# Kernel tuning notes

Hardware: AMD Instinct MI355X
Metric: run time of the kernel (lower is better)

The kernel has to match this reference:

```python
import jax, jax.numpy as jnp
import numpy as np

N_QUBITS = 8
DEPTH = 2
DIM = 2 ** N_QUBITS

# Hadamard gate (symmetric)
_H = (1.0 / np.sqrt(2.0)) * jnp.array([[1.0, 1.0], [1.0, -1.0]], dtype=jnp.complex64)
# sign table for <Z_i>: bit of wire i is bit (n-1-i) of the basis index (wire 0 = MSB)
_bits = (np.arange(DIM)[:, None] >> np.arange(N_QUBITS - 1, -1, -1)[None, :]) & 1
_SIGNS = jnp.asarray(1.0 - 2.0 * _bits, dtype=jnp.float32)  # [DIM, n_qubits]


def _quantum(ang):
    """Vectorized statevector simulation of the circuit:
    RX(ang_i) on each wire, then DEPTH x (CNOT ladder + H on last wire);
    returns <Z_i> for each wire. ang: [R, N_QUBITS] float32 -> [R, N_QUBITS]."""
    R = ang.shape[0]
    half = ang * 0.5
    a0 = jnp.cos(half).astype(jnp.complex64)
    a1 = (jnp.sin(half) * (-1j)).astype(jnp.complex64)  # RX|0> = cos|0> - i sin|1>
    single = jnp.stack([a0, a1], axis=-1)  # [R, n, 2]
    # product state via kron over qubits (wire 0 is the most significant factor)
    state = single[:, 0]  # [R, 2]
    for q in range(1, N_QUBITS):
        state = (state[:, :, None] * single[:, q][:, None, :]).reshape(R, -1)
    for _ in range(DEPTH):
        # CNOT ladder on adjacent wires (i -> i+1)
        for i in range(N_QUBITS - 1):
            s = state.reshape(R, 2 ** i, 2, 2, -1)  # [R, pre, ctrl, tgt, post]
            s = jnp.concatenate([s[:, :, :1], s[:, :, 1:, ::-1]], axis=2)
            state = s.reshape(R, -1)
        # Hadamard on the last wire
        s = state.reshape(R, -1, 2)
        state = (s @ _H).reshape(R, -1)
    probs = state.real ** 2 + state.imag ** 2  # [R, DIM]
    return probs @ _SIGNS  # [R, n_qubits]


def setup_inputs() -> dict:
    key = jax.random.key(0)
    k_x, k_w1, k_w2 = jax.random.split(key, 3)
    B, S, E, F = 8, 4096, 1024, N_QUBITS
    x = jax.random.normal(k_x, (B, S, E), dtype=jnp.float32)
    w1 = jax.random.normal(k_w1, (F, E), dtype=jnp.float32) * 0.02
    b1 = jnp.zeros((F,), dtype=jnp.float32)
    w2 = jax.random.normal(k_w2, (E, F), dtype=jnp.float32) * 0.02
    b2 = jnp.zeros((E,), dtype=jnp.float32)
    return {"x": x, "w1": w1, "b1": b1, "w2": w2, "b2": b2}


def reference(x, w1, b1, w2, b2):
    B, S, E = x.shape
    h = jnp.einsum('bse,fe->bsf', x, w1) + b1  # linear1 -> [B, S, ffn_dim]
    q = _quantum(h.reshape(-1, N_QUBITS)).reshape(B, S, N_QUBITS)
    # dropout is identity in eval mode
    return jnp.einsum('bsf,ef->bse', q, w2) + b2  # linear2 -> [B, S, E]
```

## Files before the change

kernel.cpp:

```cpp
#include <hip/hip_runtime.h>


constexpr int THREADS        = 256;
constexpr int ROWS_PER_ITER  = 8;
constexpr int ITERS          = 4;
constexpr int ROWS_PER_BLOCK = ROWS_PER_ITER * ITERS;
constexpr int E              = 1024;
constexpr int R_TOTAL        = 8 * 4096;

__global__ __launch_bounds__(THREADS)
void ffq_kernel(const float* __restrict__ x,
                const float* __restrict__ w1,
                const float* __restrict__ b1,
                const float* __restrict__ w2,
                const float* __restrict__ b2,
                float* __restrict__ out)
{
    __shared__ __align__(16) float part[2][ROWS_PER_ITER][4][8];
    __shared__ __align__(16) float qsh[2][ROWS_PER_ITER][8];
    __shared__ float b1s[8];

    const int t    = threadIdx.x;
    const int lane = t & 63;
    const int wid  = t >> 6;
    const int c0   = t * 4;

    if (t < 8) b1s[t] = b1[t];

    float4 w1r[8];
#pragma unroll
    for (int f = 0; f < 8; ++f)
        w1r[f] = *(const float4*)(w1 + f * E + c0);

    float w2a[4][8];
#pragma unroll
    for (int j = 0; j < 4; ++j) {
        const float4 lo = *(const float4*)(w2 + (size_t)(c0 + j) * 8);
        const float4 hi = *(const float4*)(w2 + (size_t)(c0 + j) * 8 + 4);
        w2a[j][0] = lo.x; w2a[j][1] = lo.y; w2a[j][2] = lo.z; w2a[j][3] = lo.w;
        w2a[j][4] = hi.x; w2a[j][5] = hi.y; w2a[j][6] = hi.z; w2a[j][7] = hi.w;
    }
    const float4 b2v = *(const float4*)(b2 + c0);

    const int row0 = blockIdx.x * ROWS_PER_BLOCK;

    float4 xv[ROWS_PER_ITER];
#pragma unroll
    for (int s = 0; s < ROWS_PER_ITER; ++s)
        xv[s] = *(const float4*)(x + (size_t)(row0 + s) * E + c0);

    for (int it = 0; it < ITERS; ++it) {
        const int p        = it & 1;
        const int rbase    = row0 + it * ROWS_PER_ITER;
        const bool hasNext = (it + 1 < ITERS);

#pragma unroll
        for (int s = 0; s < ROWS_PER_ITER; ++s) {
            const float4 xc = xv[s];
            if (hasNext)
                xv[s] = *(const float4*)(x + (size_t)(rbase + ROWS_PER_ITER + s) * E + c0);

            float h[8];
#pragma unroll
            for (int f = 0; f < 8; ++f)
                h[f] = xc.x * w1r[f].x + xc.y * w1r[f].y
                     + xc.z * w1r[f].z + xc.w * w1r[f].w;

            {   const bool hb = lane & 1;
                float s0 = hb ? h[0] : h[4];
                float s1 = hb ? h[1] : h[5];
                float s2 = hb ? h[2] : h[6];
                float s3 = hb ? h[3] : h[7];
                s0 = __shfl_xor(s0, 1); s1 = __shfl_xor(s1, 1);
                s2 = __shfl_xor(s2, 1); s3 = __shfl_xor(s3, 1);
                h[0] = (hb ? h[4] : h[0]) + s0;
                h[1] = (hb ? h[5] : h[1]) + s1;
                h[2] = (hb ? h[6] : h[2]) + s2;
                h[3] = (hb ? h[7] : h[3]) + s3;
            }
            {   const bool hb = lane & 2;
                float s0 = hb ? h[0] : h[2];
                float s1 = hb ? h[1] : h[3];
                s0 = __shfl_xor(s0, 2); s1 = __shfl_xor(s1, 2);
                h[0] = (hb ? h[2] : h[0]) + s0;
                h[1] = (hb ? h[3] : h[1]) + s1;
            }
            float v;
            {   const bool hb = lane & 4;
                float s0 = hb ? h[0] : h[1];
                s0 = __shfl_xor(s0, 4);
                v = (hb ? h[1] : h[0]) + s0;
            }
            v += __shfl_xor(v, 8);
            v += __shfl_xor(v, 16);
            v += __shfl_xor(v, 32);

            if (lane < 8) {
                const int f = ((lane & 1) << 2) | (lane & 2) | ((lane >> 2) & 1);
                part[p][s][wid][f] = v;
            }
        }
        __syncthreads();

        if (t < ROWS_PER_ITER) {
            float hq[8];
#pragma unroll
            for (int f = 0; f < 8; ++f)
                hq[f] = part[p][t][0][f] + part[p][t][1][f]
                      + part[p][t][2][f] + part[p][t][3][f] + b1s[f];
            float c[8];
#pragma unroll
            for (int f = 0; f < 8; ++f) c[f] = __cosf(hq[f]);
            const float e1 = c[0],      o1 = c[1];
            const float e2 = e1 * c[2], o2 = o1 * c[3];
            const float e3 = e2 * c[4], o3 = o2 * c[5];
            const float e4 = e3 * c[6];
            float* qp = qsh[p][t];
            qp[0] = e1; qp[1] = o1; qp[2] = e2; qp[3] = o2;
            qp[4] = e3; qp[5] = o3; qp[6] = e4; qp[7] = e4 * o3 * c[7];
        }
        __syncthreads();

#pragma unroll
        for (int s = 0; s < ROWS_PER_ITER; ++s) {
            const float4 qlo = *(const float4*)(&qsh[p][s][0]);
            const float4 qhi = *(const float4*)(&qsh[p][s][4]);
            const float qv[8] = {qlo.x, qlo.y, qlo.z, qlo.w,
                                 qhi.x, qhi.y, qhi.z, qhi.w};
            float4 o = b2v;
#pragma unroll
            for (int f = 0; f < 8; ++f) {
                o.x += qv[f] * w2a[0][f];
                o.y += qv[f] * w2a[1][f];
                o.z += qv[f] * w2a[2][f];
                o.w += qv[f] * w2a[3][f];
            }
            *(float4*)(out + (size_t)(rbase + s) * E + c0) = o;
        }
    }
}

extern "C" void kernel_launch(void* const* d_in, const int* in_sizes, int n_in,
                              void* d_out, int out_size, void* d_ws, size_t ws_size,
                              hipStream_t stream)
{
    const float* x  = (const float*)d_in[0];
    const float* w1 = (const float*)d_in[1];
    const float* b1 = (const float*)d_in[2];
    const float* w2 = (const float*)d_in[3];
    const float* b2 = (const float*)d_in[4];
    float* out = (float*)d_out;

    dim3 grid(R_TOTAL / ROWS_PER_BLOCK);
    ffq_kernel<<<grid, THREADS, 0, stream>>>(x, w1, b1, w2, b2, out);
}
```

Measured before the change: 249.5 us.

## Split fused kernel into read-reduce-cosine kernel and output-projection kernel

The single fused kernel is split in two. The first kernel streams x, computes the 8 projections and the cosine products, and writes the small q tensor to workspace. The second kernel reads q and writes the full output. The goal is to separate the read-bound phase from the write-bound phase so neither waits on the other's barriers. The cosine products are now computed in parallel across lanes with shuffle prefix products, where before a handful of threads did them. The cost is a second launch and a small round trip through global memory for q.

```diff
diff --git a/kernel.cpp b/kernel.cpp
--- a/kernel.cpp
+++ b/kernel.cpp
@@ -1,36 +1,107 @@
 #include <hip/hip_runtime.h>
 
 
-constexpr int THREADS        = 256;
-constexpr int ROWS_PER_ITER  = 8;
-constexpr int ITERS          = 4;
-constexpr int ROWS_PER_BLOCK = ROWS_PER_ITER * ITERS;
-constexpr int E              = 1024;
-constexpr int R_TOTAL        = 8 * 4096;
+constexpr int E       = 1024;
+constexpr int R_TOTAL = 8 * 4096;
+constexpr int ROWS_A  = 32;
+constexpr int ROWS_B  = 16;
 
-__global__ __launch_bounds__(THREADS)
-void ffq_kernel(const float* __restrict__ x,
-                const float* __restrict__ w1,
-                const float* __restrict__ b1,
-                const float* __restrict__ w2,
-                const float* __restrict__ b2,
-                float* __restrict__ out)
+__global__ __launch_bounds__(256)
+void ffq_qkernel(const float* __restrict__ x,
+                 const float* __restrict__ w1,
+                 const float* __restrict__ b1,
+                 float* __restrict__ q)
 {
-    __shared__ __align__(16) float part[2][ROWS_PER_ITER][4][8];
-    __shared__ __align__(16) float qsh[2][ROWS_PER_ITER][8];
-    __shared__ float b1s[8];
+    __shared__ float part[ROWS_A][33];
 
     const int t    = threadIdx.x;
     const int lane = t & 63;
     const int wid  = t >> 6;
     const int c0   = t * 4;
 
-    if (t < 8) b1s[t] = b1[t];
-
     float4 w1r[8];
 #pragma unroll
     for (int f = 0; f < 8; ++f)
         w1r[f] = *(const float4*)(w1 + f * E + c0);
+
+    const int row0 = blockIdx.x * ROWS_A;
+
+    float4 xv = *(const float4*)(x + (size_t)row0 * E + c0);
+    for (int s = 0; s < ROWS_A; ++s) {
+        const float4 xc = xv;
+        if (s + 1 < ROWS_A)
+            xv = *(const float4*)(x + (size_t)(row0 + s + 1) * E + c0);
+
+        float h[8];
+#pragma unroll
+        for (int f = 0; f < 8; ++f)
+            h[f] = xc.x * w1r[f].x + xc.y * w1r[f].y
+                 + xc.z * w1r[f].z + xc.w * w1r[f].w;
+
+        {   const bool hb = lane & 1;
+            float s0 = hb ? h[0] : h[4];
+            float s1 = hb ? h[1] : h[5];
+            float s2 = hb ? h[2] : h[6];
+            float s3 = hb ? h[3] : h[7];
+            s0 = __shfl_xor(s0, 1); s1 = __shfl_xor(s1, 1);
+            s2 = __shfl_xor(s2, 1); s3 = __shfl_xor(s3, 1);
+            h[0] = (hb ? h[4] : h[0]) + s0;
+            h[1] = (hb ? h[5] : h[1]) + s1;
+            h[2] = (hb ? h[6] : h[2]) + s2;
+            h[3] = (hb ? h[7] : h[3]) + s3;
+        }
+        {   const bool hb = lane & 2;
+            float s0 = hb ? h[0] : h[2];
+            float s1 = hb ? h[1] : h[3];
+            s0 = __shfl_xor(s0, 2); s1 = __shfl_xor(s1, 2);
+            h[0] = (hb ? h[2] : h[0]) + s0;
+            h[1] = (hb ? h[3] : h[1]) + s1;
+        }
+        float v;
+        {   const bool hb = lane & 4;
+            float s0 = hb ? h[0] : h[1];
+            s0 = __shfl_xor(s0, 4);
+            v = (hb ? h[1] : h[0]) + s0;
+        }
+        v += __shfl_xor(v, 8);
+        v += __shfl_xor(v, 16);
+        v += __shfl_xor(v, 32);
+
+        if (lane < 8) {
+            const int f = ((lane & 1) << 2) | (lane & 2) | ((lane >> 2) & 1);
+            part[s][f * 4 + wid] = v;
+        }
+    }
+    __syncthreads();
+
+    {
+        const int s = wid * 8 + (lane >> 3);
+        const int f = lane & 7;
+        const float hq = part[s][f * 4 + 0] + part[s][f * 4 + 1]
+                       + part[s][f * 4 + 2] + part[s][f * 4 + 3] + b1[f];
+        float p = __cosf(hq);
+        float u = __shfl_up(p, 2, 8); if (f >= 2) p *= u;
+        u = __shfl_up(p, 4, 8);       if (f >= 4) p *= u;
+        const float p6 = __shfl(p, 6, 8);
+        if (f == 7) p *= p6;
+        q[(size_t)(row0 + s) * 8 + f] = p;
+    }
+}
+
+__global__ __launch_bounds__(256)
+void ffq_okernel(const float* __restrict__ q,
+                 const float* __restrict__ w2,
+                 const float* __restrict__ b2,
+                 float* __restrict__ out)
+{
+    __shared__ __align__(16) float4 qsh[ROWS_B * 2];
+
+    const int t  = threadIdx.x;
+    const int c0 = t * 4;
+    const int row0 = blockIdx.x * ROWS_B;
+
+    if (t < ROWS_B * 2)
+        qsh[t] = ((const float4*)(q + (size_t)row0 * 8))[t];
 
     float w2a[4][8];
 #pragma unroll
@@ -42,101 +113,23 @@
     }
     const float4 b2v = *(const float4*)(b2 + c0);
 
-    const int row0 = blockIdx.x * ROWS_PER_BLOCK;
+    __syncthreads();
 
-    float4 xv[ROWS_PER_ITER];
+#pragma unroll 4
+    for (int s = 0; s < ROWS_B; ++s) {
+        const float4 qlo = qsh[2 * s];
+        const float4 qhi = qsh[2 * s + 1];
+        const float qv[8] = {qlo.x, qlo.y, qlo.z, qlo.w,
+                             qhi.x, qhi.y, qhi.z, qhi.w};
+        float4 o = b2v;
 #pragma unroll
-    for (int s = 0; s < ROWS_PER_ITER; ++s)
-        xv[s] = *(const float4*)(x + (size_t)(row0 + s) * E + c0);
-
-    for (int it = 0; it < ITERS; ++it) {
-        const int p        = it & 1;
-        const int rbase    = row0 + it * ROWS_PER_ITER;
-        const bool hasNext = (it + 1 < ITERS);
-
-#pragma unroll
-        for (int s = 0; s < ROWS_PER_ITER; ++s) {
-            const float4 xc = xv[s];
-            if (hasNext)
-                xv[s] = *(const float4*)(x + (size_t)(rbase + ROWS_PER_ITER + s) * E + c0);
-
-            float h[8];
-#pragma unroll
-            for (int f = 0; f < 8; ++f)
-                h[f] = xc.x * w1r[f].x + xc.y * w1r[f].y
-                     + xc.z * w1r[f].z + xc.w * w1r[f].w;
-
-            {   const bool hb = lane & 1;
-                float s0 = hb ? h[0] : h[4];
-                float s1 = hb ? h[1] : h[5];
-                float s2 = hb ? h[2] : h[6];
-                float s3 = hb ? h[3] : h[7];
-                s0 = __shfl_xor(s0, 1); s1 = __shfl_xor(s1, 1);
-                s2 = __shfl_xor(s2, 1); s3 = __shfl_xor(s3, 1);
-                h[0] = (hb ? h[4] : h[0]) + s0;
-                h[1] = (hb ? h[5] : h[1]) + s1;
-                h[2] = (hb ? h[6] : h[2]) + s2;
-                h[3] = (hb ? h[7] : h[3]) + s3;
-            }
-            {   const bool hb = lane & 2;
-                float s0 = hb ? h[0] : h[2];
-                float s1 = hb ? h[1] : h[3];
-                s0 = __shfl_xor(s0, 2); s1 = __shfl_xor(s1, 2);
-                h[0] = (hb ? h[2] : h[0]) + s0;
-                h[1] = (hb ? h[3] : h[1]) + s1;
-            }
-            float v;
-            {   const bool hb = lane & 4;
-                float s0 = hb ? h[0] : h[1];
-                s0 = __shfl_xor(s0, 4);
-                v = (hb ? h[1] : h[0]) + s0;
-            }
-            v += __shfl_xor(v, 8);
-            v += __shfl_xor(v, 16);
-            v += __shfl_xor(v, 32);
-
-            if (lane < 8) {
-                const int f = ((lane & 1) << 2) | (lane & 2) | ((lane >> 2) & 1);
-                part[p][s][wid][f] = v;
-            }
+        for (int f = 0; f < 8; ++f) {
+            o.x += qv[f] * w2a[0][f];
+            o.y += qv[f] * w2a[1][f];
+            o.z += qv[f] * w2a[2][f];
+            o.w += qv[f] * w2a[3][f];
         }
-        __syncthreads();
-
-        if (t < ROWS_PER_ITER) {
-            float hq[8];
-#pragma unroll
-            for (int f = 0; f < 8; ++f)
-                hq[f] = part[p][t][0][f] + part[p][t][1][f]
-                      + part[p][t][2][f] + part[p][t][3][f] + b1s[f];
-            float c[8];
-#pragma unroll
-            for (int f = 0; f < 8; ++f) c[f] = __cosf(hq[f]);
-            const float e1 = c[0],      o1 = c[1];
-            const float e2 = e1 * c[2], o2 = o1 * c[3];
-            const float e3 = e2 * c[4], o3 = o2 * c[5];
-            const float e4 = e3 * c[6];
-            float* qp = qsh[p][t];
-            qp[0] = e1; qp[1] = o1; qp[2] = e2; qp[3] = o2;
-            qp[4] = e3; qp[5] = o3; qp[6] = e4; qp[7] = e4 * o3 * c[7];
-        }
-        __syncthreads();
-
-#pragma unroll
-        for (int s = 0; s < ROWS_PER_ITER; ++s) {
-            const float4 qlo = *(const float4*)(&qsh[p][s][0]);
-            const float4 qhi = *(const float4*)(&qsh[p][s][4]);
-            const float qv[8] = {qlo.x, qlo.y, qlo.z, qlo.w,
-                                 qhi.x, qhi.y, qhi.z, qhi.w};
-            float4 o = b2v;
-#pragma unroll
-            for (int f = 0; f < 8; ++f) {
-                o.x += qv[f] * w2a[0][f];
-                o.y += qv[f] * w2a[1][f];
-                o.z += qv[f] * w2a[2][f];
-                o.w += qv[f] * w2a[3][f];
-            }
-            *(float4*)(out + (size_t)(rbase + s) * E + c0) = o;
-        }
+        *(float4*)(out + (size_t)(row0 + s) * E + c0) = o;
     }
 }
 
@@ -150,7 +143,8 @@
     const float* w2 = (const float*)d_in[3];
     const float* b2 = (const float*)d_in[4];
     float* out = (float*)d_out;
+    float* q   = (float*)d_ws;
 
-    dim3 grid(R_TOTAL / ROWS_PER_BLOCK);
-    ffq_kernel<<<grid, THREADS, 0, stream>>>(x, w1, b1, w2, b2, out);
+    ffq_qkernel<<<dim3(R_TOTAL / ROWS_A), 256, 0, stream>>>(x, w1, b1, q);
+    ffq_okernel<<<dim3(R_TOTAL / ROWS_B), 256, 0, stream>>>(q, w2, b2, out);
 }
```

Result: slower. 270.6 us (+8.5%).
